# Kernel tuning notes

Hardware: AMD Instinct MI355X
Metric: run time of the kernel (lower is better)

## Reference

```python
import jax, jax.numpy as jnp
import numpy as np

B, T, IN, H, OUT = 32, 1024, 256, 768, 128


def setup_inputs() -> dict:
    key = jax.random.key(0)
    ks = jax.random.split(key, 11)
    s = 0.05
    return {
        "x": jax.random.normal(ks[0], (B, T, IN), dtype=jnp.float32),
        "W_ih0": jax.random.normal(ks[1], (4 * H, IN), dtype=jnp.float32) * s,
        "W_hh0": jax.random.normal(ks[2], (4 * H, H), dtype=jnp.float32) * s,
        "b_ih0": jax.random.normal(ks[3], (4 * H,), dtype=jnp.float32) * s,
        "b_hh0": jax.random.normal(ks[4], (4 * H,), dtype=jnp.float32) * s,
        "W_ih1": jax.random.normal(ks[5], (4 * H, H), dtype=jnp.float32) * s,
        "W_hh1": jax.random.normal(ks[6], (4 * H, H), dtype=jnp.float32) * s,
        "b_ih1": jax.random.normal(ks[7], (4 * H,), dtype=jnp.float32) * s,
        "b_hh1": jax.random.normal(ks[8], (4 * H,), dtype=jnp.float32) * s,
        "W_lin": jax.random.normal(ks[9], (OUT, H), dtype=jnp.float32) * s,
        "b_lin": jax.random.normal(ks[10], (OUT,), dtype=jnp.float32) * s,
    }


def _lstm_layer(x_btd, W_ih, W_hh, b_ih, b_hh):
    # Input-side GEMM for all timesteps at once: [B,T,4H]
    xg = jnp.einsum("btd,gd->btg", x_btd, W_ih) + b_ih + b_hh
    xg = jnp.swapaxes(xg, 0, 1)  # time-major [T,B,4H]
    h0 = jnp.zeros((x_btd.shape[0], W_hh.shape[1]), x_btd.dtype)

    def step(carry, gx):
        h, c = carry
        g = gx + h @ W_hh.T  # [B,4H]
        i, f, gg, o = jnp.split(g, 4, axis=-1)  # PyTorch gate order i,f,g,o
        i, f, o = jax.nn.sigmoid(i), jax.nn.sigmoid(f), jax.nn.sigmoid(o)
        c = f * c + i * jnp.tanh(gg)
        h = o * jnp.tanh(c)
        return (h, c), h

    _, hs = jax.lax.scan(step, (h0, h0), xg)  # hs: [T,B,H]
    return jnp.swapaxes(hs, 0, 1)  # [B,T,H]


def reference(x, W_ih0, W_hh0, b_ih0, b_hh0, W_ih1, W_hh1, b_ih1, b_hh1, W_lin, b_lin):
    h1 = _lstm_layer(x, W_ih0, W_hh0, b_ih0, b_hh0)
    h2 = _lstm_layer(h1, W_ih1, W_hh1, b_ih1, b_hh1)  # eval mode: inter-layer dropout off
    return jnp.einsum("bth,oh->bto", h2, W_lin) + b_lin
```

## Files before the change

kernel.cpp:

```cpp
#include <hip/hip_runtime.h>

#define Tt    1024
#define INF   256
#define Hh    768
#define OUTF  128

#define NWG_L0  48
#define NWG_L1  48
#define NWG_LIN 2
#define NWG     (NWG_L0 + NWG_L1 + NWG_LIN)
#define NTHR    1024

typedef unsigned int       u32;
typedef unsigned long long u64;
typedef unsigned short     u16;
typedef __attribute__((ext_vector_type(8))) short bf16x8;
typedef __attribute__((ext_vector_type(4))) float f32x4;

#define PROG_OFF 0
#define HA_OFF   16384
#define HB_OFF   (HA_OFF + 3*49152)
#define WS_BYTES (HB_OFF + 3*49152)
#define HPS      24576

#define ASTR_B 1552
#define RSLAB  272
#define RROW   17

__device__ __forceinline__ float sigf(float v){ return 1.0f/(1.0f+__expf(-v)); }
__device__ __forceinline__ float tanhfast(float x){
    const float cx = fminf(fmaxf(x, -15.f), 15.f);
    const float e  = __expf(2.f * cx);
    return (e - 1.f) / (e + 1.f);
}
__device__ __forceinline__ u16 f2bf(float f){
    u32 u = __float_as_uint(f);
    return (u16)((u + 0x7fffu + ((u>>16)&1u)) >> 16);
}
__device__ __forceinline__ void st32ws(u16* p, u32 v){
    __hip_atomic_store((u32*)p, v, __ATOMIC_RELAXED, __HIP_MEMORY_SCOPE_AGENT);
}
__device__ __forceinline__ u32 ldu32(const u32* p){
    return __hip_atomic_load(p, __ATOMIC_RELAXED, __HIP_MEMORY_SCOPE_AGENT);
}
__device__ __forceinline__ void stu32(u32* p, u32 v){
    __hip_atomic_store(p, v, __ATOMIC_RELAXED, __HIP_MEMORY_SCOPE_AGENT);
}
__device__ __forceinline__ void ld16x3(const u16* p0, const u16* p1, const u16* p2,
                                       f32x4& r0, f32x4& r1, f32x4& r2){
    asm volatile(
        "global_load_dwordx4 %0, %3, off sc0 sc1\n\t"
        "global_load_dwordx4 %1, %4, off sc0 sc1\n\t"
        "global_load_dwordx4 %2, %5, off sc0 sc1\n\t"
        "s_waitcnt vmcnt(0)"
        : "=&v"(r0), "=&v"(r1), "=&v"(r2)
        : "v"(p0), "v"(p1), "v"(p2)
        : "memory");
}
__device__ __forceinline__ void ld16x6(const u16* p0, const u16* p1, const u16* p2,
                                       const u16* p3, const u16* p4, const u16* p5,
                                       f32x4& r0, f32x4& r1, f32x4& r2,
                                       f32x4& r3, f32x4& r4, f32x4& r5){
    asm volatile(
        "global_load_dwordx4 %0, %6, off sc0 sc1\n\t"
        "global_load_dwordx4 %1, %7, off sc0 sc1\n\t"
        "global_load_dwordx4 %2, %8, off sc0 sc1\n\t"
        "global_load_dwordx4 %3, %9, off sc0 sc1\n\t"
        "global_load_dwordx4 %4, %10, off sc0 sc1\n\t"
        "global_load_dwordx4 %5, %11, off sc0 sc1\n\t"
        "s_waitcnt vmcnt(0)"
        : "=&v"(r0), "=&v"(r1), "=&v"(r2), "=&v"(r3), "=&v"(r4), "=&v"(r5)
        : "v"(p0), "v"(p1), "v"(p2), "v"(p3), "v"(p4), "v"(p5)
        : "memory");
}

__device__ __forceinline__ void waitlines(u32* prog, int base, int cnt, u32 thr, int lane){
    bool ok = (lane >= cnt);
    int guard = 0;
    while (guard < (1 << 24)) {
        if (!ok) ok = (ldu32(prog + (base + lane) * 32) >= thr);
        if (__ballot(ok) == ~0ull) break;
        __builtin_amdgcn_s_sleep(1);
        ++guard;
    }
}

__global__ void prologue(char* ws){
    int i = blockIdx.x * 256 + threadIdx.x;
    if (i < WS_BYTES / 4)
        __hip_atomic_store(((u32*)ws) + i, 0u, __ATOMIC_RELAXED, __HIP_MEMORY_SCOPE_AGENT);
}

__device__ __forceinline__ bf16x8 load8w(const float* p){
    float4 v0 = *(const float4*)(p);
    float4 v1 = *(const float4*)(p + 4);
    bf16x8 r;
    r[0]=(short)f2bf(v0.x); r[1]=(short)f2bf(v0.y); r[2]=(short)f2bf(v0.z); r[3]=(short)f2bf(v0.w);
    r[4]=(short)f2bf(v1.x); r[5]=(short)f2bf(v1.y); r[6]=(short)f2bf(v1.z); r[7]=(short)f2bf(v1.w);
    return r;
}

__global__ __launch_bounds__(NTHR) void lstm_persist(
    const float* __restrict__ x,
    const float* __restrict__ Wih0, const float* __restrict__ Whh0,
    const float* __restrict__ bih0, const float* __restrict__ bhh0,
    const float* __restrict__ Wih1, const float* __restrict__ Whh1,
    const float* __restrict__ bih1, const float* __restrict__ bhh1,
    const float* __restrict__ Wlin, const float* __restrict__ blin,
    float* __restrict__ out, char* ws)
{
    u32* prog = (u32*)(ws + PROG_OFF);
    u16* hA   = (u16*)(ws + HA_OFF);
    u16* hB   = (u16*)(ws + HB_OFF);

    const int wg  = blockIdx.x;
    const int tid = threadIdx.x;

    __shared__ __align__(16) char smem[49664];
    char*  actb = smem;
    float* red  = (float*)smem;

    const int lane = tid & 63, w = tid >> 6;
    const int quad = lane >> 4, nl = lane & 15;
    const int nt = w >> 2, ks = w & 3;
    const int b3 = tid >> 5, q = tid & 31;

    const int role  = (wg < NWG_L0) ? 0 : ((wg < NWG_L0 + NWG_L1) ? 1 : 2);
    const int jbase = (role == 0) ? wg * 16 : ((role == 1) ? (wg - NWG_L0) * 16 : 0);
    const int obase = (role == 2) ? (wg - NWG_L0 - NWG_L1) * 64 : 0;

    bf16x8 bfr[12];
    if (role == 0) {
        const int grow = nt * Hh + jbase + nl;
        #pragma unroll
        for (int fi = 0; fi < 8; ++fi) {
            const int c = fi >> 2, fc = fi & 3;
            const int ka = c * 512 + ks * 128 + fc * 32 + quad * 8;
            const float* p = (ka < 256) ? (Wih0 + (size_t)grow * 256 + ka)
                                        : (Whh0 + (size_t)grow * 768 + (ka - 256));
            bfr[fi] = load8w(p);
        }
    } else if (role == 1) {
        const int grow = nt * Hh + jbase + nl;
        #pragma unroll
        for (int fi = 0; fi < 12; ++fi) {
            const int c = fi / 6, fc = fi % 6;
            const int ka = c * 768 + ks * 192 + fc * 32 + quad * 8;
            const float* p = (ka < 768) ? (Wih1 + (size_t)grow * 768 + ka)
                                        : (Whh1 + (size_t)grow * 768 + (ka - 768));
            bfr[fi] = load8w(p);
        }
    } else {
        const int row = obase + nt * 16 + nl;
        #pragma unroll
        for (int fi = 0; fi < 6; ++fi) {
            const int ka = ks * 192 + fi * 32 + quad * 8;
            bfr[fi] = load8w(Wlin + (size_t)row * 768 + ka);
        }
    }

    float ba0=0,ba1=0,ba2=0,ba3=0, bb0=0,bb1=0,bb2=0,bb3=0, creg0=0, creg1=0;
    float bl0 = 0.f, bl1 = 0.f;
    if (role < 2 && tid < 256) {
        const int jg0 = jbase + 2 * (tid >> 5), jg1 = jg0 + 1;
        const float* bi = (role == 0) ? bih0 : bih1;
        const float* bh = (role == 0) ? bhh0 : bhh1;
        ba0 = bi[jg0]        + bh[jg0];        bb0 = bi[jg1]        + bh[jg1];
        ba1 = bi[768 + jg0]  + bh[768 + jg0];  bb1 = bi[768 + jg1]  + bh[768 + jg1];
        ba2 = bi[1536 + jg0] + bh[1536 + jg0]; bb2 = bi[1536 + jg1] + bh[1536 + jg1];
        ba3 = bi[2304 + jg0] + bh[2304 + jg0]; bb3 = bi[2304 + jg1] + bh[2304 + jg1];
    }
    if (role == 2) {
        bl0 = blin[obase + (tid >> 5)];
        bl1 = blin[obase + 32 + (tid >> 5)];
    }

    for (int s = 0; s < Tt + 2; ++s) {
        const bool active = (role == 0) ? (s < Tt)
                          : (role == 1) ? (s >= 1 && s <= Tt)
                          :               (s >= 2);
        const int par_wA = s % 3;
        const int par_rA = (s + 2) % 3;
        const int par_wB = (s + 2) % 3;
        const int par_rB = (s + 1) % 3;

        if (active && w == 0) {
            if (role == 0) {
                if (s >= 1) waitlines(prog, 0, 48, (u32)s, lane);
                if (s >= 2) waitlines(prog, 48, 48, (u32)(s - 1), lane);
            } else if (role == 1) {
                waitlines(prog, 48, 48, (u32)s, lane);
                {
                    const u32 thr2 = (lane < 48) ? (u32)s : (u32)(s - 1);
                    const int idx  = (lane < 48) ? lane : (96 + (lane - 48));
                    bool ok = (lane >= 50);
                    int guard = 0;
                    while (guard < (1 << 24)) {
                        if (!ok) ok = (ldu32(prog + idx * 32) >= thr2);
                        if (__ballot(ok) == ~0ull) break;
                        __builtin_amdgcn_s_sleep(1);
                        ++guard;
                    }
                }
            } else {
                waitlines(prog, 48, 48, (u32)s, lane);
            }
        }
        __syncthreads();

        if (active) {
            f32x4 acc0 = {0.f,0.f,0.f,0.f}, acc1 = {0.f,0.f,0.f,0.f};

            if (role == 0) {
                const float* xs = x + ((size_t)b3 * Tt + s) * INF + q * 8;
                const float4 v0 = *(const float4*)xs;
                const float4 v1 = *(const float4*)(xs + 4);
                const u16* hp = hA + (size_t)par_rA * HPS + b3 * 768;
                f32x4 h0, h1, h2;
                ld16x3(hp + q * 8, hp + 256 + q * 8, hp + 512 + q * 8, h0, h1, h2);
                {
                    uint4 xv;
                    xv.x = (u32)f2bf(v0.x) | ((u32)f2bf(v0.y) << 16);
                    xv.y = (u32)f2bf(v0.z) | ((u32)f2bf(v0.w) << 16);
                    xv.z = (u32)f2bf(v1.x) | ((u32)f2bf(v1.y) << 16);
                    xv.w = (u32)f2bf(v1.z) | ((u32)f2bf(v1.w) << 16);
                    *(uint4*)(actb + b3 * ASTR_B + q * 16) = xv;
                    *(f32x4*)(actb + b3 * ASTR_B + 512 + q * 16) = h0;
                }
                __syncthreads();
                #pragma unroll
                for (int fc = 0; fc < 4; ++fc) {
                    const int koff = ks * 128 + fc * 32 + quad * 8;
                    bf16x8 a0 = *(const bf16x8*)(actb + nl * ASTR_B + koff * 2);
                    bf16x8 a1 = *(const bf16x8*)(actb + (16 + nl) * ASTR_B + koff * 2);
                    acc0 = __builtin_amdgcn_mfma_f32_16x16x32_bf16(a0, bfr[fc], acc0, 0, 0, 0);
                    acc1 = __builtin_amdgcn_mfma_f32_16x16x32_bf16(a1, bfr[fc], acc1, 0, 0, 0);
                }
                __syncthreads();
                *(f32x4*)(actb + b3 * ASTR_B + q * 16)       = h1;
                *(f32x4*)(actb + b3 * ASTR_B + 512 + q * 16) = h2;
                __syncthreads();
                #pragma unroll
                for (int fc = 0; fc < 4; ++fc) {
                    const int koff = ks * 128 + fc * 32 + quad * 8;
                    bf16x8 a0 = *(const bf16x8*)(actb + nl * ASTR_B + koff * 2);
                    bf16x8 a1 = *(const bf16x8*)(actb + (16 + nl) * ASTR_B + koff * 2);
                    acc0 = __builtin_amdgcn_mfma_f32_16x16x32_bf16(a0, bfr[4 + fc], acc0, 0, 0, 0);
                    acc1 = __builtin_amdgcn_mfma_f32_16x16x32_bf16(a1, bfr[4 + fc], acc1, 0, 0, 0);
                }
                __syncthreads();
            } else if (role == 1) {
                const u16* pA = hA + (size_t)par_rA * HPS + b3 * 768;
                const u16* pB = hB + (size_t)par_rB * HPS + b3 * 768;
                f32x4 a0, a1, a2, bq0, bq1, bq2;
                ld16x6(pA + q * 8, pA + 256 + q * 8, pA + 512 + q * 8,
                       pB + q * 8, pB + 256 + q * 8, pB + 512 + q * 8,
                       a0, a1, a2, bq0, bq1, bq2);
                *(f32x4*)(actb + b3 * ASTR_B + q * 16)        = a0;
                *(f32x4*)(actb + b3 * ASTR_B + 512 + q * 16)  = a1;
                *(f32x4*)(actb + b3 * ASTR_B + 1024 + q * 16) = a2;
                __syncthreads();
                #pragma unroll
                for (int fc = 0; fc < 6; ++fc) {
                    const int koff = ks * 192 + fc * 32 + quad * 8;
                    bf16x8 f0 = *(const bf16x8*)(actb + nl * ASTR_B + koff * 2);
                    bf16x8 f1 = *(const bf16x8*)(actb + (16 + nl) * ASTR_B + koff * 2);
                    acc0 = __builtin_amdgcn_mfma_f32_16x16x32_bf16(f0, bfr[fc], acc0, 0, 0, 0);
                    acc1 = __builtin_amdgcn_mfma_f32_16x16x32_bf16(f1, bfr[fc], acc1, 0, 0, 0);
                }
                __syncthreads();
                *(f32x4*)(actb + b3 * ASTR_B + q * 16)        = bq0;
                *(f32x4*)(actb + b3 * ASTR_B + 512 + q * 16)  = bq1;
                *(f32x4*)(actb + b3 * ASTR_B + 1024 + q * 16) = bq2;
                __syncthreads();
                #pragma unroll
                for (int fc = 0; fc < 6; ++fc) {
                    const int koff = ks * 192 + fc * 32 + quad * 8;
                    bf16x8 f0 = *(const bf16x8*)(actb + nl * ASTR_B + koff * 2);
                    bf16x8 f1 = *(const bf16x8*)(actb + (16 + nl) * ASTR_B + koff * 2);
                    acc0 = __builtin_amdgcn_mfma_f32_16x16x32_bf16(f0, bfr[6 + fc], acc0, 0, 0, 0);
                    acc1 = __builtin_amdgcn_mfma_f32_16x16x32_bf16(f1, bfr[6 + fc], acc1, 0, 0, 0);
                }
                __syncthreads();
            } else {
                const u16* pB = hB + (size_t)par_rB * HPS + b3 * 768;
                f32x4 bq0, bq1, bq2;
                ld16x3(pB + q * 8, pB + 256 + q * 8, pB + 512 + q * 8, bq0, bq1, bq2);
                *(f32x4*)(actb + b3 * ASTR_B + q * 16)        = bq0;
                *(f32x4*)(actb + b3 * ASTR_B + 512 + q * 16)  = bq1;
                *(f32x4*)(actb + b3 * ASTR_B + 1024 + q * 16) = bq2;
                __syncthreads();
                #pragma unroll
                for (int fc = 0; fc < 6; ++fc) {
                    const int koff = ks * 192 + fc * 32 + quad * 8;
                    bf16x8 f0 = *(const bf16x8*)(actb + nl * ASTR_B + koff * 2);
                    bf16x8 f1 = *(const bf16x8*)(actb + (16 + nl) * ASTR_B + koff * 2);
                    acc0 = __builtin_amdgcn_mfma_f32_16x16x32_bf16(f0, bfr[fc], acc0, 0, 0, 0);
                    acc1 = __builtin_amdgcn_mfma_f32_16x16x32_bf16(f1, bfr[fc], acc1, 0, 0, 0);
                }
                __syncthreads();
            }

            *(f32x4*)(red + (size_t)((nt * 2 + 0) * 4 + ks) * RSLAB + nl * RROW + quad * 4) = acc0;
            *(f32x4*)(red + (size_t)((nt * 2 + 1) * 4 + ks) * RSLAB + nl * RROW + quad * 4) = acc1;
            __syncthreads();

            if (role == 2) {
                const int r2 = tid >> 5, bb = tid & 31;
                const int mtr = bb >> 4, mr = bb & 15;
                const int nt0 = r2 >> 4, nr0 = r2 & 15;
                const int nt1 = (r2 + 32) >> 4, nr1 = (r2 + 32) & 15;
                float s0 = 0.f, s1 = 0.f;
                #pragma unroll
                for (int k2 = 0; k2 < 4; ++k2) {
                    s0 += red[(size_t)((nt0 * 2 + mtr) * 4 + k2) * RSLAB + nr0 * RROW + mr];
                    s1 += red[(size_t)((nt1 * 2 + mtr) * 4 + k2) * RSLAB + nr1 * RROW + mr];
                }
                const int v = s - 2;
                float* o = out + ((size_t)bb * Tt + v) * OUTF + obase;
                o[r2]      = s0 + bl0;
                o[32 + r2] = s1 + bl1;
            } else if (tid < 256) {
                const int jj = tid >> 5, b2 = tid & 31;
                const int mt = b2 >> 4, mr = b2 & 15;
                const int j0 = 2 * jj, j1 = 2 * jj + 1;
                float p0a=0,p1a=0,p2a=0,p3a=0, p0b=0,p1b=0,p2b=0,p3b=0;
                #pragma unroll
                for (int k2 = 0; k2 < 4; ++k2) {
                    p0a += red[(size_t)((0 * 2 + mt) * 4 + k2) * RSLAB + j0 * RROW + mr];
                    p1a += red[(size_t)((1 * 2 + mt) * 4 + k2) * RSLAB + j0 * RROW + mr];
                    p2a += red[(size_t)((2 * 2 + mt) * 4 + k2) * RSLAB + j0 * RROW + mr];
                    p3a += red[(size_t)((3 * 2 + mt) * 4 + k2) * RSLAB + j0 * RROW + mr];
                    p0b += red[(size_t)((0 * 2 + mt) * 4 + k2) * RSLAB + j1 * RROW + mr];
                    p1b += red[(size_t)((1 * 2 + mt) * 4 + k2) * RSLAB + j1 * RROW + mr];
                    p2b += red[(size_t)((2 * 2 + mt) * 4 + k2) * RSLAB + j1 * RROW + mr];
                    p3b += red[(size_t)((3 * 2 + mt) * 4 + k2) * RSLAB + j1 * RROW + mr];
                }
                const float ig0 = sigf(ba0 + p0a), fg0 = sigf(ba1 + p1a);
                const float gv0 = tanhfast(ba2 + p2a), og0 = sigf(ba3 + p3a);
                creg0 = fg0 * creg0 + ig0 * gv0;
                const float h0 = og0 * tanhfast(creg0);
                const float ig1 = sigf(bb0 + p0b), fg1 = sigf(bb1 + p1b);
                const float gv1 = tanhfast(bb2 + p2b), og1 = sigf(bb3 + p3b);
                creg1 = fg1 * creg1 + ig1 * gv1;
                const float h1 = og1 * tanhfast(creg1);
                u16* dst = (role == 0) ? (hA + (size_t)par_wA * HPS)
                                       : (hB + (size_t)par_wB * HPS);
                st32ws(dst + b2 * 768 + jbase + j0, (u32)f2bf(h0) | ((u32)f2bf(h1) << 16));
            }
        }

        __syncthreads();
        if (tid == 0) stu32(prog + wg * 32, (u32)(s + 1));
    }
}

extern "C" void kernel_launch(void* const* d_in, const int* in_sizes, int n_in,
                              void* d_out, int out_size, void* d_ws, size_t ws_size,
                              hipStream_t stream)
{
    const float* x    = (const float*)d_in[0];
    const float* Wih0 = (const float*)d_in[1];
    const float* Whh0 = (const float*)d_in[2];
    const float* bih0 = (const float*)d_in[3];
    const float* bhh0 = (const float*)d_in[4];
    const float* Wih1 = (const float*)d_in[5];
    const float* Whh1 = (const float*)d_in[6];
    const float* bih1 = (const float*)d_in[7];
    const float* bhh1 = (const float*)d_in[8];
    const float* Wlin = (const float*)d_in[9];
    const float* blin = (const float*)d_in[10];
    float* out = (float*)d_out;
    char*  ws  = (char*)d_ws;

    hipLaunchKernelGGL(prologue, dim3(304), dim3(256), 0, stream, ws);
    hipLaunchKernelGGL(lstm_persist, dim3(NWG), dim3(NTHR), 0, stream,
                       x, Wih0, Whh0, bih0, bhh0,
                       Wih1, Whh1, bih1, bhh1,
                       Wlin, blin, out, ws);
}
```

Before: 6.240 ms.

## Stage full activation rows in LDS once per step and merge progress waits

```diff
diff --git a/kernel.cpp b/kernel.cpp
--- a/kernel.cpp
+++ b/kernel.cpp
@@ -10,22 +10,29 @@
 #define NWG_LIN 2
 #define NWG     (NWG_L0 + NWG_L1 + NWG_LIN)
 #define NTHR    1024
+#define NIT     (Tt + 2)
 
 typedef unsigned int       u32;
-typedef unsigned long long u64;
 typedef unsigned short     u16;
 typedef __attribute__((ext_vector_type(8))) short bf16x8;
 typedef __attribute__((ext_vector_type(4))) float f32x4;
 
 #define PROG_OFF 0
+#define HPS      24576
 #define HA_OFF   16384
-#define HB_OFF   (HA_OFF + 3*49152)
-#define WS_BYTES (HB_OFF + 3*49152)
-#define HPS      24576
-
-#define ASTR_B 1552
+#define HB_OFF   (HA_OFF + 3 * 49152)
+#define WS_BYTES (HB_OFF + 3 * 49152)
+
+#define AST0   2064
+#define AST1   3088
+#define AST2   1552
+#define ACT0_B (32 * AST0)
+#define ACT1_B (32 * AST1)
+#define ACT2_B (32 * AST2)
 #define RSLAB  272
 #define RROW   17
+#define RED_B  (32 * RSLAB * 4)
+#define LDS_B  (ACT1_B + RED_B)
 
 __device__ __forceinline__ float sigf(float v){ return 1.0f/(1.0f+__expf(-v)); }
 __device__ __forceinline__ float tanhfast(float x){
@@ -74,17 +81,6 @@
         : "memory");
 }
 
-__device__ __forceinline__ void waitlines(u32* prog, int base, int cnt, u32 thr, int lane){
-    bool ok = (lane >= cnt);
-    int guard = 0;
-    while (guard < (1 << 24)) {
-        if (!ok) ok = (ldu32(prog + (base + lane) * 32) >= thr);
-        if (__ballot(ok) == ~0ull) break;
-        __builtin_amdgcn_s_sleep(1);
-        ++guard;
-    }
-}
-
 __global__ void prologue(char* ws){
     int i = blockIdx.x * 256 + threadIdx.x;
     if (i < WS_BYTES / 4)
@@ -100,7 +96,7 @@
     return r;
 }
 
-__global__ __launch_bounds__(NTHR) void lstm_persist(
+__global__ __launch_bounds__(NTHR, 4) void lstm_persist(
     const float* __restrict__ x,
     const float* __restrict__ Wih0, const float* __restrict__ Whh0,
     const float* __restrict__ bih0, const float* __restrict__ bhh0,
@@ -116,26 +112,25 @@
     const int wg  = blockIdx.x;
     const int tid = threadIdx.x;
 
-    __shared__ __align__(16) char smem[49664];
-    char*  actb = smem;
-    float* red  = (float*)smem;
+    extern __shared__ __align__(16) char smem[];
 
     const int lane = tid & 63, w = tid >> 6;
     const int quad = lane >> 4, nl = lane & 15;
     const int nt = w >> 2, ks = w & 3;
-    const int b3 = tid >> 5, q = tid & 31;
 
     const int role  = (wg < NWG_L0) ? 0 : ((wg < NWG_L0 + NWG_L1) ? 1 : 2);
     const int jbase = (role == 0) ? wg * 16 : ((role == 1) ? (wg - NWG_L0) * 16 : 0);
     const int obase = (role == 2) ? (wg - NWG_L0 - NWG_L1) * 64 : 0;
+
+    char*  actb = smem;
+    float* red  = (float*)(smem + ((role == 0) ? ACT0_B : (role == 1) ? ACT1_B : ACT2_B));
 
     bf16x8 bfr[12];
     if (role == 0) {
         const int grow = nt * Hh + jbase + nl;
         #pragma unroll
         for (int fi = 0; fi < 8; ++fi) {
-            const int c = fi >> 2, fc = fi & 3;
-            const int ka = c * 512 + ks * 128 + fc * 32 + quad * 8;
+            const int ka = ks * 256 + fi * 32 + quad * 8;
             const float* p = (ka < 256) ? (Wih0 + (size_t)grow * 256 + ka)
                                         : (Whh0 + (size_t)grow * 768 + (ka - 256));
             bfr[fi] = load8w(p);
@@ -144,8 +139,7 @@
         const int grow = nt * Hh + jbase + nl;
         #pragma unroll
         for (int fi = 0; fi < 12; ++fi) {
-            const int c = fi / 6, fc = fi % 6;
-            const int ka = c * 768 + ks * 192 + fc * 32 + quad * 8;
+            const int ka = ks * 384 + fi * 32 + quad * 8;
             const float* p = (ka < 768) ? (Wih1 + (size_t)grow * 768 + ka)
                                         : (Whh1 + (size_t)grow * 768 + (ka - 768));
             bfr[fi] = load8w(p);
@@ -175,151 +169,155 @@
         bl1 = blin[obase + 32 + (tid >> 5)];
     }
 
-    for (int s = 0; s < Tt + 2; ++s) {
-        const bool active = (role == 0) ? (s < Tt)
-                          : (role == 1) ? (s >= 1 && s <= Tt)
-                          :               (s >= 2);
+    for (int s = 0; s < NIT; ++s) {
         const int par_wA = s % 3;
         const int par_rA = (s + 2) % 3;
         const int par_wB = (s + 2) % 3;
         const int par_rB = (s + 1) % 3;
+        const bool active = (role == 0) ? (s < Tt)
+                          : (role == 1) ? (s >= 1 && s <= Tt)
+                          :               (s >= 2);
+
+        float4 xv0, xv1;
+        const int xrow = tid >> 5, xc = tid & 31;
+        if (role == 0 && active) {
+            const float* xs = x + ((size_t)xrow * Tt + s) * INF + xc * 8;
+            xv0 = ((const float4*)xs)[0];
+            xv1 = ((const float4*)xs)[1];
+        }
 
         if (active && w == 0) {
+            int ia = -1, ib = -1; u32 ta = 0, tb = 0;
             if (role == 0) {
-                if (s >= 1) waitlines(prog, 0, 48, (u32)s, lane);
-                if (s >= 2) waitlines(prog, 48, 48, (u32)(s - 1), lane);
+                if (lane < 48) {
+                    if (s >= 1) { ia = lane;      ta = (u32)s; }
+                    if (s >= 3) { ib = 48 + lane; tb = (u32)(s - 1); }
+                }
             } else if (role == 1) {
-                waitlines(prog, 48, 48, (u32)s, lane);
-                {
-                    const u32 thr2 = (lane < 48) ? (u32)s : (u32)(s - 1);
-                    const int idx  = (lane < 48) ? lane : (96 + (lane - 48));
-                    bool ok = (lane >= 50);
-                    int guard = 0;
-                    while (guard < (1 << 24)) {
-                        if (!ok) ok = (ldu32(prog + idx * 32) >= thr2);
-                        if (__ballot(ok) == ~0ull) break;
-                        __builtin_amdgcn_s_sleep(1);
-                        ++guard;
-                    }
+                if (lane < 48) {
+                    ia = lane;      ta = (u32)s;
+                    ib = 48 + lane; tb = (s >= 2) ? (u32)s : 0u;
+                } else if (lane < 50) {
+                    ib = 48 + lane;
+                    tb = (s >= 4) ? (u32)(s - 1) : 0u;
                 }
             } else {
-                waitlines(prog, 48, 48, (u32)s, lane);
+                if (lane < 48) { ia = 48 + lane; ta = (u32)s; }
+            }
+            int guard = 0;
+            while (guard < (1 << 24)) {
+                const bool o1 = (ia < 0) || (ldu32(prog + ia * 32) >= ta);
+                const bool o2 = (ib < 0) || (ldu32(prog + ib * 32) >= tb);
+                if (__ballot(o1 && o2) == ~0ull) break;
+                __builtin_amdgcn_s_sleep(1); ++guard;
             }
         }
         __syncthreads();
 
         if (active) {
+            if (role == 0) {
+                uint4 a;
+                a.x = (u32)f2bf(xv0.x) | ((u32)f2bf(xv0.y) << 16);
+                a.y = (u32)f2bf(xv0.z) | ((u32)f2bf(xv0.w) << 16);
+                a.z = (u32)f2bf(xv1.x) | ((u32)f2bf(xv1.y) << 16);
+                a.w = (u32)f2bf(xv1.z) | ((u32)f2bf(xv1.w) << 16);
+                *(uint4*)(actb + xrow * AST0 + xc * 16) = a;
+                const u16* hsrc = hA + (size_t)par_rA * HPS;
+                const int r0 = tid / 96,  c0 = tid - r0 * 96;
+                const int G1 = 1024 + tid, r1 = G1 / 96, c1 = G1 - r1 * 96;
+                const int G2 = 2048 + tid, r2 = G2 / 96, c2 = G2 - r2 * 96;
+                f32x4 h0, h1, h2;
+                ld16x3(hsrc + (size_t)r0 * 768 + c0 * 8,
+                       hsrc + (size_t)r1 * 768 + c1 * 8,
+                       hsrc + (size_t)r2 * 768 + c2 * 8, h0, h1, h2);
+                *(f32x4*)(actb + r0 * AST0 + 512 + c0 * 16) = h0;
+                *(f32x4*)(actb + r1 * AST0 + 512 + c1 * 16) = h1;
+                *(f32x4*)(actb + r2 * AST0 + 512 + c2 * 16) = h2;
+            } else if (role == 1) {
+                const u16* pA = hA + (size_t)par_rA * HPS;
+                const u16* pB = hB + (size_t)par_rB * HPS;
+                const u16* pp[6]; u32 la[6];
+                #pragma unroll
+                for (int u = 0; u < 6; ++u) {
+                    const int G = u * 1024 + tid;
+                    const int row = G / 192, c = G - row * 192;
+                    la[u] = (u32)(row * AST1 + c * 16);
+                    pp[u] = (c < 96) ? (pA + (size_t)row * 768 + (size_t)c * 8)
+                                     : (pB + (size_t)row * 768 + (size_t)(c - 96) * 8);
+                }
+                f32x4 h0, h1, h2, h3, h4, h5;
+                ld16x6(pp[0], pp[1], pp[2], pp[3], pp[4], pp[5],
+                       h0, h1, h2, h3, h4, h5);
+                *(f32x4*)(actb + la[0]) = h0;
+                *(f32x4*)(actb + la[1]) = h1;
+                *(f32x4*)(actb + la[2]) = h2;
+                *(f32x4*)(actb + la[3]) = h3;
+                *(f32x4*)(actb + la[4]) = h4;
+                *(f32x4*)(actb + la[5]) = h5;
+            } else {
+                const u16* pB = hB + (size_t)par_rB * HPS;
+                const int r0 = tid / 96,  c0 = tid - r0 * 96;
+                const int G1 = 1024 + tid, r1 = G1 / 96, c1 = G1 - r1 * 96;
+                const int G2 = 2048 + tid, r2 = G2 / 96, c2 = G2 - r2 * 96;
+                f32x4 h0, h1, h2;
+                ld16x3(pB + (size_t)r0 * 768 + c0 * 8,
+                       pB + (size_t)r1 * 768 + c1 * 8,
+                       pB + (size_t)r2 * 768 + c2 * 8, h0, h1, h2);
+                *(f32x4*)(actb + r0 * AST2 + c0 * 16) = h0;
+                *(f32x4*)(actb + r1 * AST2 + c1 * 16) = h1;
+                *(f32x4*)(actb + r2 * AST2 + c2 * 16) = h2;
+            }
+            __syncthreads();
+
             f32x4 acc0 = {0.f,0.f,0.f,0.f}, acc1 = {0.f,0.f,0.f,0.f};
-
             if (role == 0) {
-                const float* xs = x + ((size_t)b3 * Tt + s) * INF + q * 8;
-                const float4 v0 = *(const float4*)xs;
-                const float4 v1 = *(const float4*)(xs + 4);
-                const u16* hp = hA + (size_t)par_rA * HPS + b3 * 768;
-                f32x4 h0, h1, h2;
-                ld16x3(hp + q * 8, hp + 256 + q * 8, hp + 512 + q * 8, h0, h1, h2);
-                {
-                    uint4 xv;
-                    xv.x = (u32)f2bf(v0.x) | ((u32)f2bf(v0.y) << 16);
-                    xv.y = (u32)f2bf(v0.z) | ((u32)f2bf(v0.w) << 16);
-                    xv.z = (u32)f2bf(v1.x) | ((u32)f2bf(v1.y) << 16);
-                    xv.w = (u32)f2bf(v1.z) | ((u32)f2bf(v1.w) << 16);
-                    *(uint4*)(actb + b3 * ASTR_B + q * 16) = xv;
-                    *(f32x4*)(actb + b3 * ASTR_B + 512 + q * 16) = h0;
-                }
-                __syncthreads();
-                #pragma unroll
-                for (int fc = 0; fc < 4; ++fc) {
-                    const int koff = ks * 128 + fc * 32 + quad * 8;
-                    bf16x8 a0 = *(const bf16x8*)(actb + nl * ASTR_B + koff * 2);
-                    bf16x8 a1 = *(const bf16x8*)(actb + (16 + nl) * ASTR_B + koff * 2);
+                #pragma unroll
+                for (int fc = 0; fc < 8; ++fc) {
+                    const int kb = (ks * 256 + fc * 32 + quad * 8) * 2;
+                    bf16x8 a0 = *(const bf16x8*)(actb + nl * AST0 + kb);
+                    bf16x8 a1 = *(const bf16x8*)(actb + (16 + nl) * AST0 + kb);
                     acc0 = __builtin_amdgcn_mfma_f32_16x16x32_bf16(a0, bfr[fc], acc0, 0, 0, 0);
                     acc1 = __builtin_amdgcn_mfma_f32_16x16x32_bf16(a1, bfr[fc], acc1, 0, 0, 0);
                 }
-                __syncthreads();
-                *(f32x4*)(actb + b3 * ASTR_B + q * 16)       = h1;
-                *(f32x4*)(actb + b3 * ASTR_B + 512 + q * 16) = h2;
-                __syncthreads();
-                #pragma unroll
-                for (int fc = 0; fc < 4; ++fc) {
-                    const int koff = ks * 128 + fc * 32 + quad * 8;
-                    bf16x8 a0 = *(const bf16x8*)(actb + nl * ASTR_B + koff * 2);
-                    bf16x8 a1 = *(const bf16x8*)(actb + (16 + nl) * ASTR_B + koff * 2);
-                    acc0 = __builtin_amdgcn_mfma_f32_16x16x32_bf16(a0, bfr[4 + fc], acc0, 0, 0, 0);
-                    acc1 = __builtin_amdgcn_mfma_f32_16x16x32_bf16(a1, bfr[4 + fc], acc1, 0, 0, 0);
-                }
-                __syncthreads();
             } else if (role == 1) {
-                const u16* pA = hA + (size_t)par_rA * HPS + b3 * 768;
-                const u16* pB = hB + (size_t)par_rB * HPS + b3 * 768;
-                f32x4 a0, a1, a2, bq0, bq1, bq2;
-                ld16x6(pA + q * 8, pA + 256 + q * 8, pA + 512 + q * 8,
-                       pB + q * 8, pB + 256 + q * 8, pB + 512 + q * 8,
-                       a0, a1, a2, bq0, bq1, bq2);
-                *(f32x4*)(actb + b3 * ASTR_B + q * 16)        = a0;
-                *(f32x4*)(actb + b3 * ASTR_B + 512 + q * 16)  = a1;
-                *(f32x4*)(actb + b3 * ASTR_B + 1024 + q * 16) = a2;
-                __syncthreads();
+                #pragma unroll
+                for (int fc = 0; fc < 12; ++fc) {
+                    const int kb = (ks * 384 + fc * 32 + quad * 8) * 2;
+                    bf16x8 a0 = *(const bf16x8*)(actb + nl * AST1 + kb);
+                    bf16x8 a1 = *(const bf16x8*)(actb + (16 + nl) * AST1 + kb);
+                    acc0 = __builtin_amdgcn_mfma_f32_16x16x32_bf16(a0, bfr[fc], acc0, 0, 0, 0);
+                    acc1 = __builtin_amdgcn_mfma_f32_16x16x32_bf16(a1, bfr[fc], acc1, 0, 0, 0);
+                }
+            } else {
                 #pragma unroll
                 for (int fc = 0; fc < 6; ++fc) {
-                    const int koff = ks * 192 + fc * 32 + quad * 8;
-                    bf16x8 f0 = *(const bf16x8*)(actb + nl * ASTR_B + koff * 2);
-                    bf16x8 f1 = *(const bf16x8*)(actb + (16 + nl) * ASTR_B + koff * 2);
-                    acc0 = __builtin_amdgcn_mfma_f32_16x16x32_bf16(f0, bfr[fc], acc0, 0, 0, 0);
-                    acc1 = __builtin_amdgcn_mfma_f32_16x16x32_bf16(f1, bfr[fc], acc1, 0, 0, 0);
-                }
-                __syncthreads();
-                *(f32x4*)(actb + b3 * ASTR_B + q * 16)        = bq0;
-                *(f32x4*)(actb + b3 * ASTR_B + 512 + q * 16)  = bq1;
-                *(f32x4*)(actb + b3 * ASTR_B + 1024 + q * 16) = bq2;
-                __syncthreads();
-                #pragma unroll
-                for (int fc = 0; fc < 6; ++fc) {
-                    const int koff = ks * 192 + fc * 32 + quad * 8;
-                    bf16x8 f0 = *(const bf16x8*)(actb + nl * ASTR_B + koff * 2);
-                    bf16x8 f1 = *(const bf16x8*)(actb + (16 + nl) * ASTR_B + koff * 2);
-                    acc0 = __builtin_amdgcn_mfma_f32_16x16x32_bf16(f0, bfr[6 + fc], acc0, 0, 0, 0);
-                    acc1 = __builtin_amdgcn_mfma_f32_16x16x32_bf16(f1, bfr[6 + fc], acc1, 0, 0, 0);
-                }
-                __syncthreads();
-            } else {
-                const u16* pB = hB + (size_t)par_rB * HPS + b3 * 768;
-                f32x4 bq0, bq1, bq2;
-                ld16x3(pB + q * 8, pB + 256 + q * 8, pB + 512 + q * 8, bq0, bq1, bq2);
-                *(f32x4*)(actb + b3 * ASTR_B + q * 16)        = bq0;
-                *(f32x4*)(actb + b3 * ASTR_B + 512 + q * 16)  = bq1;
-                *(f32x4*)(actb + b3 * ASTR_B + 1024 + q * 16) = bq2;
-                __syncthreads();
-                #pragma unroll
-                for (int fc = 0; fc < 6; ++fc) {
-                    const int koff = ks * 192 + fc * 32 + quad * 8;
-                    bf16x8 f0 = *(const bf16x8*)(actb + nl * ASTR_B + koff * 2);
-                    bf16x8 f1 = *(const bf16x8*)(actb + (16 + nl) * ASTR_B + koff * 2);
-                    acc0 = __builtin_amdgcn_mfma_f32_16x16x32_bf16(f0, bfr[fc], acc0, 0, 0, 0);
-                    acc1 = __builtin_amdgcn_mfma_f32_16x16x32_bf16(f1, bfr[fc], acc1, 0, 0, 0);
-                }
-                __syncthreads();
-            }
-
-            *(f32x4*)(red + (size_t)((nt * 2 + 0) * 4 + ks) * RSLAB + nl * RROW + quad * 4) = acc0;
-            *(f32x4*)(red + (size_t)((nt * 2 + 1) * 4 + ks) * RSLAB + nl * RROW + quad * 4) = acc1;
+                    const int kb = (ks * 192 + fc * 32 + quad * 8) * 2;
+                    bf16x8 a0 = *(const bf16x8*)(actb + nl * AST2 + kb);
+                    bf16x8 a1 = *(const bf16x8*)(actb + (16 + nl) * AST2 + kb);
+                    acc0 = __builtin_amdgcn_mfma_f32_16x16x32_bf16(a0, bfr[fc], acc0, 0, 0, 0);
+                    acc1 = __builtin_amdgcn_mfma_f32_16x16x32_bf16(a1, bfr[fc], acc1, 0, 0, 0);
+                }
+            }
+            *(f32x4*)&red[(size_t)((nt * 2 + 0) * 4 + ks) * RSLAB + nl * RROW + quad * 4] = acc0;
+            *(f32x4*)&red[(size_t)((nt * 2 + 1) * 4 + ks) * RSLAB + nl * RROW + quad * 4] = acc1;
             __syncthreads();
 
             if (role == 2) {
-                const int r2 = tid >> 5, bb = tid & 31;
-                const int mtr = bb >> 4, mr = bb & 15;
-                const int nt0 = r2 >> 4, nr0 = r2 & 15;
-                const int nt1 = (r2 + 32) >> 4, nr1 = (r2 + 32) & 15;
+                if (tid == 0) stu32(prog + wg * 32, (u32)(s + 1));
+                const int v = s - 2;
+                const int r2o = tid >> 5, bb = tid & 31;
+                const int mtr = bb >> 4, mr2 = bb & 15;
+                const int nt0 = r2o >> 4, nr0 = r2o & 15;
+                const int nt1 = (r2o + 32) >> 4, nr1 = (r2o + 32) & 15;
                 float s0 = 0.f, s1 = 0.f;
                 #pragma unroll
                 for (int k2 = 0; k2 < 4; ++k2) {
-                    s0 += red[(size_t)((nt0 * 2 + mtr) * 4 + k2) * RSLAB + nr0 * RROW + mr];
-                    s1 += red[(size_t)((nt1 * 2 + mtr) * 4 + k2) * RSLAB + nr1 * RROW + mr];
-                }
-                const int v = s - 2;
+                    s0 += red[(size_t)((nt0 * 2 + mtr) * 4 + k2) * RSLAB + nr0 * RROW + mr2];
+                    s1 += red[(size_t)((nt1 * 2 + mtr) * 4 + k2) * RSLAB + nr1 * RROW + mr2];
+                }
                 float* o = out + ((size_t)bb * Tt + v) * OUTF + obase;
-                o[r2]      = s0 + bl0;
-                o[32 + r2] = s1 + bl1;
+                o[r2o]      = s0 + bl0;
+                o[32 + r2o] = s1 + bl1;
             } else if (tid < 256) {
                 const int jj = tid >> 5, b2 = tid & 31;
                 const int mt = b2 >> 4, mr = b2 & 15;
@@ -346,7 +344,8 @@
                 const float h1 = og1 * tanhfast(creg1);
                 u16* dst = (role == 0) ? (hA + (size_t)par_wA * HPS)
                                        : (hB + (size_t)par_wB * HPS);
-                st32ws(dst + b2 * 768 + jbase + j0, (u32)f2bf(h0) | ((u32)f2bf(h1) << 16));
+                st32ws(dst + b2 * 768 + jbase + j0,
+                       (u32)f2bf(h0) | ((u32)f2bf(h1) << 16));
             }
         }
 
@@ -373,8 +372,15 @@
     float* out = (float*)d_out;
     char*  ws  = (char*)d_ws;
 
+    static bool attr_done = false;
+    if (!attr_done) {
+        hipFuncSetAttribute((const void*)lstm_persist,
+                            hipFuncAttributeMaxDynamicSharedMemorySize, 160 * 1024);
+        attr_done = true;
+    }
+
     hipLaunchKernelGGL(prologue, dim3(304), dim3(256), 0, stream, ws);
-    hipLaunchKernelGGL(lstm_persist, dim3(NWG), dim3(NTHR), 0, stream,
+    hipLaunchKernelGGL(lstm_persist, dim3(NWG), dim3(NTHR), LDS_B, stream,
                        x, Wih0, Whh0, bih0, bhh0,
                        Wih1, Whh1, bih1, bhh1,
                        Wlin, blin, out, ws);
```

New measurement: 7.998 ms. 1.28x slower.
